# Kernel optimization log

Hardware: AMD Instinct MI355X
Metric: run time of the kernel (lower is better)

Reference implementation:

```python
import jax, jax.numpy as jnp
import numpy as np

B, S, E, OUT = 16, 2048, 256, 256


def setup_inputs() -> dict:
    key = jax.random.key(0)
    k1, k2 = jax.random.split(key)
    x = jax.random.normal(k1, (B, S, E), dtype=jnp.float32)
    alpha = jnp.float32(0.5)  # nn.Parameter(torch.tensor(0.5))
    W = jax.random.normal(k2, (OUT, E), dtype=jnp.float32) * (1.0 / np.sqrt(E))
    b = jnp.zeros((OUT,), dtype=jnp.float32)
    return {"x": x, "alpha\u0308".replace("\u0308", ""): alpha, "W": W, "b": b}


def reference(x, alpha, W, b):
    # Gaussian energy-well self-attention: q = k = v = x, shape (B, S, E)
    # cdist(q, k, p=2)**2 == ||q||^2 + ||k||^2 - 2 q.k
    sq = jnp.sum(x * x, axis=-1)                                   # (B, S)
    d2 = sq[:, :, None] + sq[:, None, :] - 2.0 * jnp.einsum(
        "bse,bte->bst", x, x)                                      # (B, S, S)
    d2 = jnp.maximum(d2, 0.0)
    weights = jnp.exp(-alpha * d2)                                 # (B, S, S)
    weights = jax.nn.softmax(weights, axis=-1)
    attn = jnp.einsum("bst,bte->bse", weights, x)                  # (B, S, E)
    pooled = attn.mean(axis=1)                                     # (B, E)
    return pooled @ W.T + b                                        # (B, OUT)
```

## Files before the change

kernel.cpp:

```cpp
#include <hip/hip_runtime.h>
#include <hip/hip_bf16.h>

#define NB 16
#define NS 2048
#define NE 256
#define NOUT 256
#define TRI 136

typedef __attribute__((ext_vector_type(4))) float f32x4;
typedef __attribute__((ext_vector_type(8))) short s16x8;
typedef __attribute__((ext_vector_type(4))) short s16x4;
typedef unsigned int u32;

__device__ __forceinline__ short bf16rn(float f) {
  unsigned u = __builtin_bit_cast(unsigned, f);
  u += 0x7FFFu + ((u >> 16) & 1u);
  return (short)(u >> 16);
}
__device__ __forceinline__ float bf16f(short s) {
  unsigned u = ((unsigned)(unsigned short)s) << 16;
  return __builtin_bit_cast(float, u);
}
__device__ __forceinline__ void gld_lds16(const void* g, void* l) {
  __builtin_amdgcn_global_load_lds(
      (const __attribute__((address_space(1))) u32*)g,
      (__attribute__((address_space(3))) u32*)l, 16, 0, 0);
}

__global__ __launch_bounds__(256) void prep_kernel(const float* __restrict__ x,
                                                   short* __restrict__ xbf,
                                                   float* __restrict__ sq) {
  int row = blockIdx.x * 4 + (threadIdx.x >> 6);
  int lane = threadIdx.x & 63;
  f32x4 v = *(const f32x4*)(x + (size_t)row * NE + lane * 4);
  s16x4 p;
  p[0] = bf16rn(v.x); p[1] = bf16rn(v.y); p[2] = bf16rn(v.z); p[3] = bf16rn(v.w);
  *(s16x4*)(xbf + (size_t)row * NE + lane * 4) = p;
  float s = v.x * v.x + v.y * v.y + v.z * v.z + v.w * v.w;
#pragma unroll
  for (int off = 32; off; off >>= 1) s += __shfl_xor(s, off);
  if (lane == 0) sq[row] = s;
}

__global__ __launch_bounds__(256, 4) void gram1(
    const short* __restrict__ xbf, const float* __restrict__ sqg,
    const float* __restrict__ alpha_p, float* __restrict__ rws,
    int* __restrict__ flags) {
  __shared__ short ldsA[128 * 64];
  __shared__ short ldsB[128 * 64];
  __shared__ float sqs[128];
  __shared__ float sqt[128];

  const int tid = threadIdx.x;
  int bid = blockIdx.x;
  int nbid = (bid & 7) * 272 + (bid >> 3);
  int bb = nbid / 136;
  int t = nbid - bb * 136;
  int by = 0;
  while (t >= 16 - by) { t -= 16 - by; ++by; }
  int bx = by + t;
  const int rowbase = by * 128, colbase = bx * 128;
  const short* xb = xbf + (size_t)bb * NS * NE;

  if (tid < 128) {
    sqs[tid] = sqg[bb * NS + rowbase + tid];
    sqt[tid] = sqg[bb * NS + colbase + tid];
  }
  const float alpha = alpha_p[0];

  const int lane = tid & 63;
  const int wid = tid >> 6;
  const int wr = wid >> 1, wc = wid & 1;
  const int lrow = lane & 15, lq = lane >> 4;

  const int boff = ((lane & 7) * 16) ^ ((lane >> 3) << 4);
  const char* gA = (const char*)xb + (size_t)(rowbase + wid * 32 + (lane >> 3)) * 512 + boff;
  const char* gB = (const char*)xb + (size_t)(colbase + wid * 32 + (lane >> 3)) * 512 + boff;
  char* lA = (char*)ldsA + wid * 32 * 128 + lane * 16;
  char* lB = (char*)ldsB + wid * 32 * 128 + lane * 16;

  f32x4 acc[4][4];
#pragma unroll
  for (int m = 0; m < 4; ++m)
#pragma unroll
    for (int n = 0; n < 4; ++n) acc[m][n] = (f32x4){0.f, 0.f, 0.f, 0.f};

#pragma unroll 1
  for (int kt = 0; kt < 4; ++kt) {
    __syncthreads();
#pragma unroll
    for (int i = 0; i < 4; ++i) {
      gld_lds16(gA + (size_t)kt * 128 + i * 4096, lA + i * 1024);
      gld_lds16(gB + (size_t)kt * 128 + i * 4096, lB + i * 1024);
    }
    __syncthreads();
#pragma unroll
    for (int kk = 0; kk < 2; ++kk) {
      s16x8 af[4], bfv[4];
#pragma unroll
      for (int m = 0; m < 4; ++m) {
        int r = wr * 64 + m * 16 + lrow;
        int byt = r * 128 + (((kk * 64) + lq * 16) ^ ((r & 7) << 4));
        af[m] = *(const s16x8*)((const char*)ldsA + byt);
      }
#pragma unroll
      for (int n = 0; n < 4; ++n) {
        int r = wc * 64 + n * 16 + lrow;
        int byt = r * 128 + (((kk * 64) + lq * 16) ^ ((r & 7) << 4));
        bfv[n] = *(const s16x8*)((const char*)ldsB + byt);
      }
#pragma unroll
      for (int m = 0; m < 4; ++m)
#pragma unroll
        for (int n = 0; n < 4; ++n)
          acc[m][n] = __builtin_amdgcn_mfma_f32_16x16x32_bf16(af[m], bfv[n],
                                                              acc[m][n], 0, 0, 0);
    }
  }

  const float nal = -alpha;
  const float thresh = 17.328680f / alpha;
  float ssq[4][4], sqtl[4];
#pragma unroll
  for (int m = 0; m < 4; ++m)
#pragma unroll
    for (int j = 0; j < 4; ++j) ssq[m][j] = sqs[wr * 64 + m * 16 + lq * 4 + j];
#pragma unroll
  for (int n = 0; n < 4; ++n) sqtl[n] = sqt[wc * 64 + n * 16 + lrow];

  float mind2 = 3.4e38f;
#pragma unroll
  for (int m = 0; m < 4; ++m)
#pragma unroll
    for (int n = 0; n < 4; ++n)
#pragma unroll
      for (int j = 0; j < 4; ++j)
        mind2 = fminf(mind2, fmaf(-2.f, acc[m][n][j], ssq[m][j] + sqtl[n]));
  const bool skip = __all(mind2 > thresh);

  if (skip) {
    if (lrow == 0) {
#pragma unroll
      for (int m = 0; m < 4; ++m)
#pragma unroll
        for (int j = 0; j < 4; ++j)
          atomicAdd(&rws[bb * NS + rowbase + wr * 64 + m * 16 + lq * 4 + j], 64.0f);
    }
    if (by != bx && lq == 0) {
#pragma unroll
      for (int n = 0; n < 4; ++n)
        atomicAdd(&rws[bb * NS + colbase + wc * 64 + n * 16 + lrow], 64.0f);
    }
  } else {
    if (lane == 0) {
      atomicOr(&flags[bb * 256 + by * 16 + bx], 1);
      if (by != bx) atomicOr(&flags[bb * 256 + bx * 16 + by], 1);
    }
    float csum[4] = {0.f, 0.f, 0.f, 0.f};
#pragma unroll
    for (int m = 0; m < 4; ++m) {
#pragma unroll
      for (int j = 0; j < 4; ++j) {
        float rsum = 0.f;
#pragma unroll
        for (int n = 0; n < 4; ++n) {
          float d2 = fmaxf(fmaf(-2.f, acc[m][n][j], ssq[m][j] + sqtl[n]), 0.f);
          float w = __expf(__expf(nal * d2));
          rsum += w;
          csum[n] += w;
        }
        rsum += __shfl_xor(rsum, 1);
        rsum += __shfl_xor(rsum, 2);
        rsum += __shfl_xor(rsum, 4);
        rsum += __shfl_xor(rsum, 8);
        if (lrow == 0)
          atomicAdd(&rws[bb * NS + rowbase + wr * 64 + m * 16 + lq * 4 + j], rsum);
      }
    }
    if (by != bx) {
#pragma unroll
      for (int n = 0; n < 4; ++n) {
        float v = csum[n];
        v += __shfl_xor(v, 16);
        v += __shfl_xor(v, 32);
        if (lq == 0)
          atomicAdd(&rws[bb * NS + colbase + wc * 64 + n * 16 + lrow], v);
      }
    }
  }
}

__global__ __launch_bounds__(128) void rinv_kernel(const float* __restrict__ rws,
                                                   float* __restrict__ rinv_g,
                                                   float* __restrict__ rbsum) {
  __shared__ float ws2[2];
  int i = blockIdx.x * 128 + threadIdx.x;
  float inv = 1.0f / rws[i];
  rinv_g[i] = inv;
  float s = inv;
#pragma unroll
  for (int off = 32; off; off >>= 1) s += __shfl_xor(s, off);
  if ((threadIdx.x & 63) == 0) ws2[threadIdx.x >> 6] = s;
  __syncthreads();
  if (threadIdx.x == 0) rbsum[blockIdx.x] = ws2[0] + ws2[1];
}

__global__ __launch_bounds__(256, 4) void gram2(
    const short* __restrict__ xbf, const float* __restrict__ sqg,
    const float* __restrict__ alpha_p, const float* __restrict__ rinv_g,
    const float* __restrict__ rbsum, const int* __restrict__ flags,
    float* __restrict__ cws) {
  __shared__ short ldsA[128 * 64];
  __shared__ short ldsB[128 * 64];
  __shared__ float sqs[128];
  __shared__ float sqt[128];
  __shared__ float rinvs[128];

  const int tid = threadIdx.x;
  int bid = blockIdx.x;
  int nbid = (bid & 7) * 512 + (bid >> 3);
  int bb = nbid >> 8;
  int rr = nbid & 255;
  int by = rr >> 4, bx = rr & 15;
  const int rowbase = by * 128, colbase = bx * 128;

  if (flags[bb * 256 + by * 16 + bx] == 0) {
    if (tid < 128) atomicAdd(&cws[bb * NS + colbase + tid], rbsum[bb * 16 + by]);
    return;
  }

  const short* xb = xbf + (size_t)bb * NS * NE;
  if (tid < 128) {
    sqs[tid] = sqg[bb * NS + rowbase + tid];
    sqt[tid] = sqg[bb * NS + colbase + tid];
    rinvs[tid] = rinv_g[bb * NS + rowbase + tid];
  }
  const float alpha = alpha_p[0];

  const int lane = tid & 63;
  const int wid = tid >> 6;
  const int wr = wid >> 1, wc = wid & 1;
  const int lrow = lane & 15, lq = lane >> 4;

  const int boff = ((lane & 7) * 16) ^ ((lane >> 3) << 4);
  const char* gA = (const char*)xb + (size_t)(rowbase + wid * 32 + (lane >> 3)) * 512 + boff;
  const char* gB = (const char*)xb + (size_t)(colbase + wid * 32 + (lane >> 3)) * 512 + boff;
  char* lA = (char*)ldsA + wid * 32 * 128 + lane * 16;
  char* lB = (char*)ldsB + wid * 32 * 128 + lane * 16;

  f32x4 acc[4][4];
#pragma unroll
  for (int m = 0; m < 4; ++m)
#pragma unroll
    for (int n = 0; n < 4; ++n) acc[m][n] = (f32x4){0.f, 0.f, 0.f, 0.f};

#pragma unroll 1
  for (int kt = 0; kt < 4; ++kt) {
    __syncthreads();
#pragma unroll
    for (int i = 0; i < 4; ++i) {
      gld_lds16(gA + (size_t)kt * 128 + i * 4096, lA + i * 1024);
      gld_lds16(gB + (size_t)kt * 128 + i * 4096, lB + i * 1024);
    }
    __syncthreads();
#pragma unroll
    for (int kk = 0; kk < 2; ++kk) {
      s16x8 af[4], bfv[4];
#pragma unroll
      for (int m = 0; m < 4; ++m) {
        int r = wr * 64 + m * 16 + lrow;
        int byt = r * 128 + (((kk * 64) + lq * 16) ^ ((r & 7) << 4));
        af[m] = *(const s16x8*)((const char*)ldsA + byt);
      }
#pragma unroll
      for (int n = 0; n < 4; ++n) {
        int r = wc * 64 + n * 16 + lrow;
        int byt = r * 128 + (((kk * 64) + lq * 16) ^ ((r & 7) << 4));
        bfv[n] = *(const s16x8*)((const char*)ldsB + byt);
      }
#pragma unroll
      for (int m = 0; m < 4; ++m)
#pragma unroll
        for (int n = 0; n < 4; ++n)
          acc[m][n] = __builtin_amdgcn_mfma_f32_16x16x32_bf16(af[m], bfv[n],
                                                              acc[m][n], 0, 0, 0);
    }
  }

  const float nal = -alpha;
  float csum[4] = {0.f, 0.f, 0.f, 0.f};
#pragma unroll
  for (int m = 0; m < 4; ++m) {
#pragma unroll
    for (int j = 0; j < 4; ++j) {
      int rl = wr * 64 + m * 16 + lq * 4 + j;
      float ssq = sqs[rl];
      float ri = rinvs[rl];
#pragma unroll
      for (int n = 0; n < 4; ++n) {
        int cl = wc * 64 + n * 16 + lrow;
        float d2 = fmaxf(fmaf(-2.f, acc[m][n][j], ssq + sqt[cl]), 0.f);
        float w0 = __expf(nal * d2);
        csum[n] = fmaf(__expf(w0), ri, csum[n]);
      }
    }
  }
#pragma unroll
  for (int n = 0; n < 4; ++n) {
    float v = csum[n];
    v += __shfl_xor(v, 16);
    v += __shfl_xor(v, 32);
    if (lq == 0) atomicAdd(&cws[bb * NS + colbase + wc * 64 + n * 16 + lrow], v);
  }
}

__global__ __launch_bounds__(256) void pooled_kernel(const short* __restrict__ xbf,
                                                     const float* __restrict__ cws,
                                                     float* __restrict__ pooled) {
  int b = blockIdx.y;
  int t0 = blockIdx.x * 128;
  const short* xb = xbf + ((size_t)b * NS + t0) * NE;
  const float* cb = cws + b * NS + t0;
  float acc = 0.f;
#pragma unroll 4
  for (int t = 0; t < 128; ++t)
    acc = fmaf(cb[t], bf16f(xb[(size_t)t * NE + threadIdx.x]), acc);
  atomicAdd(&pooled[b * NE + threadIdx.x], acc * (1.0f / NS));
}

__global__ __launch_bounds__(256) void out_kernel(const float* __restrict__ pooled,
                                                  const float* __restrict__ W,
                                                  const float* __restrict__ bias,
                                                  float* __restrict__ out) {
  __shared__ float pl[NE];
  int b = blockIdx.x, o = threadIdx.x;
  pl[o] = pooled[b * NE + o];
  __syncthreads();
  const f32x4* wr4 = (const f32x4*)(W + (size_t)o * NE);
  float acc = bias[o];
#pragma unroll 8
  for (int e = 0; e < 64; ++e) {
    f32x4 w4 = wr4[e];
    acc += pl[e * 4 + 0] * w4.x + pl[e * 4 + 1] * w4.y + pl[e * 4 + 2] * w4.z +
           pl[e * 4 + 3] * w4.w;
  }
  out[b * NOUT + o] = acc;
}

extern "C" void kernel_launch(void* const* d_in, const int* in_sizes, int n_in,
                              void* d_out, int out_size, void* d_ws, size_t ws_size,
                              hipStream_t stream) {
  const float* x = (const float*)d_in[0];
  const float* alpha = (const float*)d_in[1];
  const float* W = (const float*)d_in[2];
  const float* bias = (const float*)d_in[3];
  float* out = (float*)d_out;

  float* rws = (float*)d_ws;
  float* cws = rws + NB * NS;
  float* pooled = cws + NB * NS;
  int* flags = (int*)(pooled + NB * NE);
  float* sq = (float*)(flags + NB * 256);
  float* rinv_g = sq + NB * NS;
  float* rbsum = rinv_g + NB * NS;
  short* xbf = (short*)(rbsum + NB * 16);

  hipMemsetAsync(rws, 0,
                 (size_t)(2 * NB * NS + NB * NE + NB * 256) * sizeof(float),
                 stream);

  prep_kernel<<<NB * NS / 4, 256, 0, stream>>>(x, xbf, sq);
  gram1<<<NB * TRI, 256, 0, stream>>>(xbf, sq, alpha, rws, flags);
  rinv_kernel<<<NB * 16, 128, 0, stream>>>(rws, rinv_g, rbsum);
  gram2<<<NB * 256, 256, 0, stream>>>(xbf, sq, alpha, rinv_g, rbsum, flags, cws);
  pooled_kernel<<<dim3(16, NB), 256, 0, stream>>>(xbf, cws, pooled);
  out_kernel<<<NB, 256, 0, stream>>>(pooled, W, bias, out);
}
```

Before: 157.8 us.

## Persistent double-buffered gram1, fold skipped-tile sums into init kernel, vectorize pooling

gram1 becomes a persistent-style kernel where each block processes four triangle tiles in sequence. It double-buffers the K-slices in 64KB LDS so global-to-LDS loads overlap MFMA work, and it decodes tile indices with a closed-form sqrt. gram2 also gets double buffering, and skipped tiles now exit immediately. Their contribution is precomputed by a new rinv_cinit kernel that initializes cws from the flags, which removes the separate rinv kernel and many atomics. The pooled kernel uses 16-byte vector loads with an LDS reduction. The trade-off is lower occupancy (launch bounds 2) and fewer blocks in gram1, which risks load imbalance.

```diff
diff --git a/kernel.cpp b/kernel.cpp
--- a/kernel.cpp
+++ b/kernel.cpp
@@ -5,7 +5,10 @@
 #define NS 2048
 #define NE 256
 #define NOUT 256
+#define NTILE 16
 #define TRI 136
+#define NCHUNK 544
+#define NIT 16
 
 typedef __attribute__((ext_vector_type(4))) float f32x4;
 typedef __attribute__((ext_vector_type(8))) short s16x8;
@@ -25,6 +28,60 @@
   __builtin_amdgcn_global_load_lds(
       (const __attribute__((address_space(1))) u32*)g,
       (__attribute__((address_space(3))) u32*)l, 16, 0, 0);
+}
+
+__device__ __forceinline__ void tri_decode(int T, int& by, int& bx) {
+  float f = sqrtf((float)(1089 - 8 * T));
+  int b = (int)((33.0f - f) * 0.5f);
+  if (b * (33 - b) / 2 > T) --b;
+  else if ((b + 1) * (32 - b) / 2 <= T) ++b;
+  by = b;
+  bx = b + (T - b * (33 - b) / 2);
+}
+
+__device__ __forceinline__ void stage(char* ldsbase, const short* xbf, int bb,
+                                      int rowbase, int colbase, int kt, int wid,
+                                      int lane) {
+  const char* xb = (const char*)(xbf + (size_t)bb * NS * NE);
+  const int boff = ((lane & 7) * 16) ^ (((lane >> 3) & 7) << 4);
+  const char* gA =
+      xb + (size_t)(rowbase + wid * 32 + (lane >> 3)) * 512 + boff + kt * 128;
+  const char* gB =
+      xb + (size_t)(colbase + wid * 32 + (lane >> 3)) * 512 + boff + kt * 128;
+  char* lA = ldsbase + wid * 32 * 128 + lane * 16;
+  char* lB = ldsbase + 16384 + wid * 32 * 128 + lane * 16;
+#pragma unroll
+  for (int i = 0; i < 4; ++i) {
+    gld_lds16(gA + i * 4096, lA + i * 1024);
+    gld_lds16(gB + i * 4096, lB + i * 1024);
+  }
+}
+
+__device__ __forceinline__ void compute64(const char* bufA, const char* bufB,
+                                          int wr, int wc, int lrow, int lq,
+                                          f32x4 acc[4][4]) {
+#pragma unroll
+  for (int kk = 0; kk < 2; ++kk) {
+    s16x8 af[4], bfv[4];
+#pragma unroll
+    for (int m = 0; m < 4; ++m) {
+      int r = wr * 64 + m * 16 + lrow;
+      int byt = r * 128 + (((kk * 64) + lq * 16) ^ ((r & 7) << 4));
+      af[m] = *(const s16x8*)(bufA + byt);
+    }
+#pragma unroll
+    for (int n = 0; n < 4; ++n) {
+      int r = wc * 64 + n * 16 + lrow;
+      int byt = r * 128 + (((kk * 64) + lq * 16) ^ ((r & 7) << 4));
+      bfv[n] = *(const s16x8*)(bufB + byt);
+    }
+#pragma unroll
+    for (int m = 0; m < 4; ++m)
+#pragma unroll
+      for (int n = 0; n < 4; ++n)
+        acc[m][n] = __builtin_amdgcn_mfma_f32_16x16x32_bf16(af[m], bfv[n],
+                                                            acc[m][n], 0, 0, 0);
+  }
 }
 
 __global__ __launch_bounds__(256) void prep_kernel(const float* __restrict__ x,
@@ -42,42 +99,23 @@
   if (lane == 0) sq[row] = s;
 }
 
-__global__ __launch_bounds__(256, 4) void gram1(
+__global__ __launch_bounds__(256, 2) void gram1(
     const short* __restrict__ xbf, const float* __restrict__ sqg,
     const float* __restrict__ alpha_p, float* __restrict__ rws,
     int* __restrict__ flags) {
-  __shared__ short ldsA[128 * 64];
-  __shared__ short ldsB[128 * 64];
-  __shared__ float sqs[128];
-  __shared__ float sqt[128];
+  __shared__ char lds[65536];
 
   const int tid = threadIdx.x;
-  int bid = blockIdx.x;
-  int nbid = (bid & 7) * 272 + (bid >> 3);
-  int bb = nbid / 136;
-  int t = nbid - bb * 136;
-  int by = 0;
-  while (t >= 16 - by) { t -= 16 - by; ++by; }
-  int bx = by + t;
-  const int rowbase = by * 128, colbase = bx * 128;
-  const short* xb = xbf + (size_t)bb * NS * NE;
-
-  if (tid < 128) {
-    sqs[tid] = sqg[bb * NS + rowbase + tid];
-    sqt[tid] = sqg[bb * NS + colbase + tid];
-  }
-  const float alpha = alpha_p[0];
-
   const int lane = tid & 63;
   const int wid = tid >> 6;
   const int wr = wid >> 1, wc = wid & 1;
   const int lrow = lane & 15, lq = lane >> 4;
-
-  const int boff = ((lane & 7) * 16) ^ ((lane >> 3) << 4);
-  const char* gA = (const char*)xb + (size_t)(rowbase + wid * 32 + (lane >> 3)) * 512 + boff;
-  const char* gB = (const char*)xb + (size_t)(colbase + wid * 32 + (lane >> 3)) * 512 + boff;
-  char* lA = (char*)ldsA + wid * 32 * 128 + lane * 16;
-  char* lB = (char*)ldsB + wid * 32 * 128 + lane * 16;
+  const float alpha = alpha_p[0];
+  const float nal = -alpha;
+  const float thresh = 17.328680f / alpha;
+
+  const int chunk = (blockIdx.x & 7) * 68 + (blockIdx.x >> 3);
+  const int Gbase = chunk * 4;
 
   f32x4 acc[4][4];
 #pragma unroll
@@ -85,168 +123,166 @@
 #pragma unroll
     for (int n = 0; n < 4; ++n) acc[m][n] = (f32x4){0.f, 0.f, 0.f, 0.f};
 
+  {
+    int g = Gbase, bb = g / 136, by, bx;
+    tri_decode(g - bb * 136, by, bx);
+    stage(lds, xbf, bb, by * 128, bx * 128, 0, wid, lane);
+  }
+  __syncthreads();
+
 #pragma unroll 1
-  for (int kt = 0; kt < 4; ++kt) {
-    __syncthreads();
-#pragma unroll
-    for (int i = 0; i < 4; ++i) {
-      gld_lds16(gA + (size_t)kt * 128 + i * 4096, lA + i * 1024);
-      gld_lds16(gB + (size_t)kt * 128 + i * 4096, lB + i * 1024);
+  for (int it = 0; it < NIT; ++it) {
+    const int cur = it & 1;
+    if (it + 1 < NIT) {
+      int g2 = Gbase + ((it + 1) >> 2);
+      int bb2 = g2 / 136, by2, bx2;
+      tri_decode(g2 - bb2 * 136, by2, bx2);
+      stage(lds + (cur ^ 1) * 32768, xbf, bb2, by2 * 128, bx2 * 128,
+            (it + 1) & 3, wid, lane);
+    }
+    compute64(lds + cur * 32768, lds + cur * 32768 + 16384, wr, wc, lrow, lq,
+              acc);
+
+    if ((it & 3) == 3) {
+      int g = Gbase + (it >> 2);
+      int bb = g / 136, by, bx;
+      tri_decode(g - bb * 136, by, bx);
+      const int rowbase = by * 128, colbase = bx * 128;
+      const float* sqrow = sqg + bb * NS + rowbase;
+      const float* sqcol = sqg + bb * NS + colbase;
+
+      float ssq[4][4], sqtl[4];
+#pragma unroll
+      for (int m = 0; m < 4; ++m)
+#pragma unroll
+        for (int j = 0; j < 4; ++j) ssq[m][j] = sqrow[wr * 64 + m * 16 + lq * 4 + j];
+#pragma unroll
+      for (int n = 0; n < 4; ++n) sqtl[n] = sqcol[wc * 64 + n * 16 + lrow];
+
+      float mind2 = 3.4e38f;
+#pragma unroll
+      for (int m = 0; m < 4; ++m)
+#pragma unroll
+        for (int n = 0; n < 4; ++n)
+#pragma unroll
+          for (int j = 0; j < 4; ++j)
+            mind2 = fminf(mind2, fmaf(-2.f, acc[m][n][j], ssq[m][j] + sqtl[n]));
+      const bool skip = __all(mind2 > thresh);
+
+      if (skip) {
+        if (lrow == 0) {
+#pragma unroll
+          for (int m = 0; m < 4; ++m)
+#pragma unroll
+            for (int j = 0; j < 4; ++j)
+              atomicAdd(&rws[bb * NS + rowbase + wr * 64 + m * 16 + lq * 4 + j],
+                        64.0f);
+        }
+        if (by != bx && lq == 0) {
+#pragma unroll
+          for (int n = 0; n < 4; ++n)
+            atomicAdd(&rws[bb * NS + colbase + wc * 64 + n * 16 + lrow], 64.0f);
+        }
+      } else {
+        if (lane == 0) {
+          atomicOr(&flags[bb * 256 + by * 16 + bx], 1);
+          if (by != bx) atomicOr(&flags[bb * 256 + bx * 16 + by], 1);
+        }
+        float csum[4] = {0.f, 0.f, 0.f, 0.f};
+#pragma unroll
+        for (int m = 0; m < 4; ++m) {
+#pragma unroll
+          for (int j = 0; j < 4; ++j) {
+            float rsum = 0.f;
+#pragma unroll
+            for (int n = 0; n < 4; ++n) {
+              float d2 = fmaxf(fmaf(-2.f, acc[m][n][j], ssq[m][j] + sqtl[n]), 0.f);
+              float w = __expf(__expf(nal * d2));
+              rsum += w;
+              csum[n] += w;
+            }
+            rsum += __shfl_xor(rsum, 1);
+            rsum += __shfl_xor(rsum, 2);
+            rsum += __shfl_xor(rsum, 4);
+            rsum += __shfl_xor(rsum, 8);
+            if (lrow == 0)
+              atomicAdd(&rws[bb * NS + rowbase + wr * 64 + m * 16 + lq * 4 + j],
+                        rsum);
+          }
+        }
+        if (by != bx) {
+#pragma unroll
+          for (int n = 0; n < 4; ++n) {
+            float v = csum[n];
+            v += __shfl_xor(v, 16);
+            v += __shfl_xor(v, 32);
+            if (lq == 0)
+              atomicAdd(&rws[bb * NS + colbase + wc * 64 + n * 16 + lrow], v);
+          }
+        }
+      }
+#pragma unroll
+      for (int m = 0; m < 4; ++m)
+#pragma unroll
+        for (int n = 0; n < 4; ++n) acc[m][n] = (f32x4){0.f, 0.f, 0.f, 0.f};
     }
     __syncthreads();
-#pragma unroll
-    for (int kk = 0; kk < 2; ++kk) {
-      s16x8 af[4], bfv[4];
-#pragma unroll
-      for (int m = 0; m < 4; ++m) {
-        int r = wr * 64 + m * 16 + lrow;
-        int byt = r * 128 + (((kk * 64) + lq * 16) ^ ((r & 7) << 4));
-        af[m] = *(const s16x8*)((const char*)ldsA + byt);
-      }
-#pragma unroll
-      for (int n = 0; n < 4; ++n) {
-        int r = wc * 64 + n * 16 + lrow;
-        int byt = r * 128 + (((kk * 64) + lq * 16) ^ ((r & 7) << 4));
-        bfv[n] = *(const s16x8*)((const char*)ldsB + byt);
-      }
-#pragma unroll
-      for (int m = 0; m < 4; ++m)
-#pragma unroll
-        for (int n = 0; n < 4; ++n)
-          acc[m][n] = __builtin_amdgcn_mfma_f32_16x16x32_bf16(af[m], bfv[n],
-                                                              acc[m][n], 0, 0, 0);
-    }
-  }
-
-  const float nal = -alpha;
-  const float thresh = 17.328680f / alpha;
-  float ssq[4][4], sqtl[4];
-#pragma unroll
-  for (int m = 0; m < 4; ++m)
-#pragma unroll
-    for (int j = 0; j < 4; ++j) ssq[m][j] = sqs[wr * 64 + m * 16 + lq * 4 + j];
-#pragma unroll
-  for (int n = 0; n < 4; ++n) sqtl[n] = sqt[wc * 64 + n * 16 + lrow];
-
-  float mind2 = 3.4e38f;
-#pragma unroll
-  for (int m = 0; m < 4; ++m)
-#pragma unroll
-    for (int n = 0; n < 4; ++n)
-#pragma unroll
-      for (int j = 0; j < 4; ++j)
-        mind2 = fminf(mind2, fmaf(-2.f, acc[m][n][j], ssq[m][j] + sqtl[n]));
-  const bool skip = __all(mind2 > thresh);
-
-  if (skip) {
-    if (lrow == 0) {
-#pragma unroll
-      for (int m = 0; m < 4; ++m)
-#pragma unroll
-        for (int j = 0; j < 4; ++j)
-          atomicAdd(&rws[bb * NS + rowbase + wr * 64 + m * 16 + lq * 4 + j], 64.0f);
-    }
-    if (by != bx && lq == 0) {
-#pragma unroll
-      for (int n = 0; n < 4; ++n)
-        atomicAdd(&rws[bb * NS + colbase + wc * 64 + n * 16 + lrow], 64.0f);
-    }
-  } else {
-    if (lane == 0) {
-      atomicOr(&flags[bb * 256 + by * 16 + bx], 1);
-      if (by != bx) atomicOr(&flags[bb * 256 + bx * 16 + by], 1);
-    }
-    float csum[4] = {0.f, 0.f, 0.f, 0.f};
-#pragma unroll
-    for (int m = 0; m < 4; ++m) {
-#pragma unroll
-      for (int j = 0; j < 4; ++j) {
-        float rsum = 0.f;
-#pragma unroll
-        for (int n = 0; n < 4; ++n) {
-          float d2 = fmaxf(fmaf(-2.f, acc[m][n][j], ssq[m][j] + sqtl[n]), 0.f);
-          float w = __expf(__expf(nal * d2));
-          rsum += w;
-          csum[n] += w;
-        }
-        rsum += __shfl_xor(rsum, 1);
-        rsum += __shfl_xor(rsum, 2);
-        rsum += __shfl_xor(rsum, 4);
-        rsum += __shfl_xor(rsum, 8);
-        if (lrow == 0)
-          atomicAdd(&rws[bb * NS + rowbase + wr * 64 + m * 16 + lq * 4 + j], rsum);
-      }
-    }
-    if (by != bx) {
-#pragma unroll
-      for (int n = 0; n < 4; ++n) {
-        float v = csum[n];
-        v += __shfl_xor(v, 16);
-        v += __shfl_xor(v, 32);
-        if (lq == 0)
-          atomicAdd(&rws[bb * NS + colbase + wc * 64 + n * 16 + lrow], v);
-      }
-    }
-  }
-}
-
-__global__ __launch_bounds__(128) void rinv_kernel(const float* __restrict__ rws,
-                                                   float* __restrict__ rinv_g,
-                                                   float* __restrict__ rbsum) {
-  __shared__ float ws2[2];
-  int i = blockIdx.x * 128 + threadIdx.x;
-  float inv = 1.0f / rws[i];
-  rinv_g[i] = inv;
-  float s = inv;
-#pragma unroll
-  for (int off = 32; off; off >>= 1) s += __shfl_xor(s, off);
-  if ((threadIdx.x & 63) == 0) ws2[threadIdx.x >> 6] = s;
-  __syncthreads();
-  if (threadIdx.x == 0) rbsum[blockIdx.x] = ws2[0] + ws2[1];
-}
-
-__global__ __launch_bounds__(256, 4) void gram2(
+  }
+}
+
+__global__ __launch_bounds__(256) void rinv_cinit(const float* __restrict__ rws,
+                                                  const int* __restrict__ flags,
+                                                  float* __restrict__ rinv_g,
+                                                  float* __restrict__ cws) {
+  __shared__ float rb[16];
+  const int b = blockIdx.x, tid = threadIdx.x;
+  const int lane = tid & 63;
+  if (tid < 16) rb[tid] = 0.f;
+  __syncthreads();
+#pragma unroll
+  for (int k = 0; k < 8; ++k) {
+    int r = tid + k * 256;
+    float inv = 1.0f / rws[b * NS + r];
+    rinv_g[b * NS + r] = inv;
+    float s = inv;
+#pragma unroll
+    for (int off = 32; off; off >>= 1) s += __shfl_xor(s, off);
+    if (lane == 0) atomicAdd(&rb[r >> 7], s);
+  }
+  __syncthreads();
+#pragma unroll
+  for (int k = 0; k < 8; ++k) {
+    int t = tid + k * 256;
+    int bx = t >> 7;
+    float base = 0.f;
+#pragma unroll
+    for (int by = 0; by < 16; ++by)
+      if (flags[b * 256 + by * 16 + bx] == 0) base += rb[by];
+    cws[b * NS + t] = base;
+  }
+}
+
+__global__ __launch_bounds__(256, 2) void gram2(
     const short* __restrict__ xbf, const float* __restrict__ sqg,
     const float* __restrict__ alpha_p, const float* __restrict__ rinv_g,
-    const float* __restrict__ rbsum, const int* __restrict__ flags,
-    float* __restrict__ cws) {
-  __shared__ short ldsA[128 * 64];
-  __shared__ short ldsB[128 * 64];
-  __shared__ float sqs[128];
-  __shared__ float sqt[128];
-  __shared__ float rinvs[128];
-
+    const int* __restrict__ flags, float* __restrict__ cws) {
+  __shared__ char lds[65536];
+
+  const int bid = blockIdx.x;
+  const int nbid = (bid & 7) * 512 + (bid >> 3);
+  const int bb = nbid >> 8;
+  const int rr = nbid & 255;
+  const int by = rr >> 4, bx = rr & 15;
+  if (flags[bb * 256 + by * 16 + bx] == 0) return;
+
+  const int rowbase = by * 128, colbase = bx * 128;
   const int tid = threadIdx.x;
-  int bid = blockIdx.x;
-  int nbid = (bid & 7) * 512 + (bid >> 3);
-  int bb = nbid >> 8;
-  int rr = nbid & 255;
-  int by = rr >> 4, bx = rr & 15;
-  const int rowbase = by * 128, colbase = bx * 128;
-
-  if (flags[bb * 256 + by * 16 + bx] == 0) {
-    if (tid < 128) atomicAdd(&cws[bb * NS + colbase + tid], rbsum[bb * 16 + by]);
-    return;
-  }
-
-  const short* xb = xbf + (size_t)bb * NS * NE;
-  if (tid < 128) {
-    sqs[tid] = sqg[bb * NS + rowbase + tid];
-    sqt[tid] = sqg[bb * NS + colbase + tid];
-    rinvs[tid] = rinv_g[bb * NS + rowbase + tid];
-  }
-  const float alpha = alpha_p[0];
-
   const int lane = tid & 63;
   const int wid = tid >> 6;
   const int wr = wid >> 1, wc = wid & 1;
   const int lrow = lane & 15, lq = lane >> 4;
-
-  const int boff = ((lane & 7) * 16) ^ ((lane >> 3) << 4);
-  const char* gA = (const char*)xb + (size_t)(rowbase + wid * 32 + (lane >> 3)) * 512 + boff;
-  const char* gB = (const char*)xb + (size_t)(colbase + wid * 32 + (lane >> 3)) * 512 + boff;
-  char* lA = (char*)ldsA + wid * 32 * 128 + lane * 16;
-  char* lB = (char*)ldsB + wid * 32 * 128 + lane * 16;
+  const float alpha = alpha_p[0];
+  const float nal = -alpha;
 
   f32x4 acc[4][4];
 #pragma unroll
@@ -254,52 +290,32 @@
 #pragma unroll
     for (int n = 0; n < 4; ++n) acc[m][n] = (f32x4){0.f, 0.f, 0.f, 0.f};
 
+  stage(lds, xbf, bb, rowbase, colbase, 0, wid, lane);
+  __syncthreads();
 #pragma unroll 1
-  for (int kt = 0; kt < 4; ++kt) {
+  for (int it = 0; it < 4; ++it) {
+    const int cur = it & 1;
+    if (it + 1 < 4)
+      stage(lds + (cur ^ 1) * 32768, xbf, bb, rowbase, colbase, it + 1, wid, lane);
+    compute64(lds + cur * 32768, lds + cur * 32768 + 16384, wr, wc, lrow, lq,
+              acc);
     __syncthreads();
-#pragma unroll
-    for (int i = 0; i < 4; ++i) {
-      gld_lds16(gA + (size_t)kt * 128 + i * 4096, lA + i * 1024);
-      gld_lds16(gB + (size_t)kt * 128 + i * 4096, lB + i * 1024);
-    }
-    __syncthreads();
-#pragma unroll
-    for (int kk = 0; kk < 2; ++kk) {
-      s16x8 af[4], bfv[4];
-#pragma unroll
-      for (int m = 0; m < 4; ++m) {
-        int r = wr * 64 + m * 16 + lrow;
-        int byt = r * 128 + (((kk * 64) + lq * 16) ^ ((r & 7) << 4));
-        af[m] = *(const s16x8*)((const char*)ldsA + byt);
-      }
-#pragma unroll
-      for (int n = 0; n < 4; ++n) {
-        int r = wc * 64 + n * 16 + lrow;
-        int byt = r * 128 + (((kk * 64) + lq * 16) ^ ((r & 7) << 4));
-        bfv[n] = *(const s16x8*)((const char*)ldsB + byt);
-      }
-#pragma unroll
-      for (int m = 0; m < 4; ++m)
-#pragma unroll
-        for (int n = 0; n < 4; ++n)
-          acc[m][n] = __builtin_amdgcn_mfma_f32_16x16x32_bf16(af[m], bfv[n],
-                                                              acc[m][n], 0, 0, 0);
-    }
-  }
-
-  const float nal = -alpha;
+  }
+
+  const float* sqrow = sqg + bb * NS + rowbase;
+  const float* sqcol = sqg + bb * NS + colbase;
+  const float* rirow = rinv_g + bb * NS + rowbase;
   float csum[4] = {0.f, 0.f, 0.f, 0.f};
 #pragma unroll
   for (int m = 0; m < 4; ++m) {
 #pragma unroll
     for (int j = 0; j < 4; ++j) {
       int rl = wr * 64 + m * 16 + lq * 4 + j;
-      float ssq = sqs[rl];
-      float ri = rinvs[rl];
+      float ssq = sqrow[rl];
+      float ri = rirow[rl];
 #pragma unroll
       for (int n = 0; n < 4; ++n) {
-        int cl = wc * 64 + n * 16 + lrow;
-        float d2 = fmaxf(fmaf(-2.f, acc[m][n][j], ssq + sqt[cl]), 0.f);
+        float d2 = fmaxf(fmaf(-2.f, acc[m][n][j], ssq + sqcol[wc * 64 + n * 16 + lrow]), 0.f);
         float w0 = __expf(nal * d2);
         csum[n] = fmaf(__expf(w0), ri, csum[n]);
       }
@@ -317,15 +333,28 @@
 __global__ __launch_bounds__(256) void pooled_kernel(const short* __restrict__ xbf,
                                                      const float* __restrict__ cws,
                                                      float* __restrict__ pooled) {
-  int b = blockIdx.y;
-  int t0 = blockIdx.x * 128;
+  __shared__ float red[8 * 256];
+  const int b = blockIdx.y;
+  const int t0 = blockIdx.x * 128;
   const short* xb = xbf + ((size_t)b * NS + t0) * NE;
   const float* cb = cws + b * NS + t0;
-  float acc = 0.f;
+  const int g = threadIdx.x >> 5;
+  const int e8 = (threadIdx.x & 31) * 8;
+  float acc[8] = {0.f, 0.f, 0.f, 0.f, 0.f, 0.f, 0.f, 0.f};
 #pragma unroll 4
-  for (int t = 0; t < 128; ++t)
-    acc = fmaf(cb[t], bf16f(xb[(size_t)t * NE + threadIdx.x]), acc);
-  atomicAdd(&pooled[b * NE + threadIdx.x], acc * (1.0f / NS));
+  for (int t = g; t < 128; t += 8) {
+    float cv = cb[t];
+    s16x8 v = *(const s16x8*)(xb + (size_t)t * NE + e8);
+#pragma unroll
+    for (int j = 0; j < 8; ++j) acc[j] = fmaf(cv, bf16f(v[j]), acc[j]);
+  }
+#pragma unroll
+  for (int j = 0; j < 8; ++j) red[g * 256 + e8 + j] = acc[j];
+  __syncthreads();
+  float s = 0.f;
+#pragma unroll
+  for (int g2 = 0; g2 < 8; ++g2) s += red[g2 * 256 + threadIdx.x];
+  atomicAdd(&pooled[b * NE + threadIdx.x], s * (1.0f / NS));
 }
 
 __global__ __launch_bounds__(256) void out_kernel(const float* __restrict__ pooled,
@@ -357,22 +386,20 @@
   float* out = (float*)d_out;
 
   float* rws = (float*)d_ws;
-  float* cws = rws + NB * NS;
-  float* pooled = cws + NB * NS;
+  float* pooled = rws + NB * NS;
   int* flags = (int*)(pooled + NB * NE);
-  float* sq = (float*)(flags + NB * 256);
+  float* cws = (float*)(flags + NB * 256);
+  float* sq = cws + NB * NS;
   float* rinv_g = sq + NB * NS;
-  float* rbsum = rinv_g + NB * NS;
-  short* xbf = (short*)(rbsum + NB * 16);
-
-  hipMemsetAsync(rws, 0,
-                 (size_t)(2 * NB * NS + NB * NE + NB * 256) * sizeof(float),
+  short* xbf = (short*)(rinv_g + NB * NS);
+
+  hipMemsetAsync(rws, 0, (size_t)(NB * NS + NB * NE + NB * 256) * sizeof(float),
                  stream);
 
   prep_kernel<<<NB * NS / 4, 256, 0, stream>>>(x, xbf, sq);
-  gram1<<<NB * TRI, 256, 0, stream>>>(xbf, sq, alpha, rws, flags);
-  rinv_kernel<<<NB * 16, 128, 0, stream>>>(rws, rinv_g, rbsum);
-  gram2<<<NB * 256, 256, 0, stream>>>(xbf, sq, alpha, rinv_g, rbsum, flags, cws);
+  gram1<<<NCHUNK, 256, 0, stream>>>(xbf, sq, alpha, rws, flags);
+  rinv_cinit<<<NB, 256, 0, stream>>>(rws, flags, rinv_g, cws);
+  gram2<<<NB * 256, 256, 0, stream>>>(xbf, sq, alpha, rinv_g, flags, cws);
   pooled_kernel<<<dim3(16, NB), 256, 0, stream>>>(xbf, cws, pooled);
   out_kernel<<<NB, 256, 0, stream>>>(pooled, W, bias, out);
 }
```

New measurement: 169.1 us. 7.2% more time.
